# Kernel tuning notes

Measured on AMD Instinct MI355X. Metric: run time of the kernel, lower is better.

The kernel has to match this reference:

```python
import jax, jax.numpy as jnp
import numpy as np

F = 256          # in_features
T = 8            # num_fragment_ion_types = 4 types * 2 charges
N_MONO, N_CLEAV, N_FRAG, N_OUT = 150000, 100000, 80000, 40000
D_CLEAV, D_JOIN, D_COMB = 4, 2, 4


def setup_inputs() -> dict:
    key = jax.random.key(0)
    ks = jax.random.split(key, 14)
    s = 0.05
    return {
        "feature": jax.random.normal(ks[0], (N_MONO, F), jnp.float32),
        "Wg_lost": jax.random.normal(ks[1], (F, 1), jnp.float32) * s,
        "Wg_ret": jax.random.normal(ks[2], (F, 1), jnp.float32) * s,
        "W_ih": jax.random.normal(ks[3], (4 * F, 2 * F), jnp.float32) * s,
        "W_hh": jax.random.normal(ks[4], (4 * F, F), jnp.float32) * s,
        "b_ih": jax.random.normal(ks[5], (4 * F,), jnp.float32) * s,
        "b_hh": jax.random.normal(ks[6], (4 * F,), jnp.float32) * s,
        "Wg_frag": jax.random.normal(ks[7], (F, 1), jnp.float32) * s,
        "W_out": jax.random.normal(ks[8], (F, T), jnp.float32) * s,
        "b_out": jnp.zeros((T,), jnp.float32),
        "lost_src": jax.random.randint(ks[9], (N_CLEAV, D_CLEAV), 0, N_MONO),
        "retained_src": jax.random.randint(ks[10], (N_CLEAV, D_CLEAV), 0, N_MONO),
        "join_src": jax.random.randint(ks[11], (N_FRAG, D_JOIN), 0, N_CLEAV),
        "combine_src": jax.random.randint(ks[12], (N_OUT, D_COMB), 0, N_FRAG),
    }


def _attention_sum(h, Wg):
    # h: [N, D, F] mailbox; gate = Linear(F,1,no bias); softmax over neighbor axis
    logits = jnp.einsum('ndf,fo->ndo', h, Wg)          # [N, D, 1]
    a = jax.nn.softmax(logits, axis=1)
    return jnp.sum(a * h, axis=1)                       # [N, F]


def _lstm(x, W_ih, W_hh, b_ih, b_hh):
    # x: [N, L, I]; torch nn.LSTM gate order i,f,g,o; zero initial state
    N = x.shape[0]
    H = W_hh.shape[1]
    def step(carry, xt):
        h, c = carry
        gates = xt @ W_ih.T + h @ W_hh.T + b_ih + b_hh  # [N, 4H]
        i, f, g, o = jnp.split(gates, 4, axis=-1)
        c = jax.nn.sigmoid(f) * c + jax.nn.sigmoid(i) * jnp.tanh(g)
        h = jax.nn.sigmoid(o) * jnp.tanh(c)
        return (h, c), h
    init = (jnp.zeros((N, H), x.dtype), jnp.zeros((N, H), x.dtype))
    _, hs = jax.lax.scan(step, init, jnp.swapaxes(x, 0, 1))
    return jnp.swapaxes(hs, 0, 1)                       # [N, L, H]


def reference(feature, Wg_lost, Wg_ret, W_ih, W_hh, b_ih, b_hh,
              Wg_frag, W_out, b_out,
              lost_src, retained_src, join_src, combine_src):
    h_lost = _attention_sum(feature[lost_src], Wg_lost)        # [N_cleav, F]
    h_ret = _attention_sum(feature[retained_src], Wg_ret)      # [N_cleav, F]
    cleav = jnp.concatenate([h_lost, h_ret], axis=-1)          # [N_cleav, 2F]
    # Fragment pull over 'join' edges: LSTM over neighbor set, then attention sum
    hs = _lstm(cleav[join_src], W_ih, W_hh, b_ih, b_hh)        # [N_frag, D_join, F]
    frag = _attention_sum(hs, Wg_frag)                         # [N_frag, F]
    # Output head: Linear + ReLU
    frag_out = jax.nn.relu(frag @ W_out + b_out)               # [N_frag, T]
    # copy_u_sum over 'combine' edges: scatter-sum of src outputs to dst
    return frag_out[combine_src].sum(axis=1)                   # [N_out, T]
```

## Files before the change

kernel.cpp:

```cpp
#include <hip/hip_runtime.h>

typedef unsigned short u16;
typedef unsigned int u32;
typedef float f32x4 __attribute__((ext_vector_type(4)));
typedef __bf16 bf16x8 __attribute__((ext_vector_type(8)));

#define F 256
#define T_OUT 8
#define N_MONO 150000
#define N_CLEAV 100000
#define N_FRAG 80000
#define N_OUT 40000
#define M_CLEAV_PAD 100352

static __device__ __forceinline__ u16 f2bf(float f) {
  u32 u = __float_as_uint(f);
  u32 r = (u + 0x7FFFu + ((u >> 16) & 1u)) >> 16;
  return (u16)r;
}
static __device__ __forceinline__ float bf2f(u16 b) {
  return __uint_as_float(((u32)b) << 16);
}
static __device__ __forceinline__ float sigmoidf(float x) {
  return __frcp_rn(1.0f + __expf(-x));
}
static __device__ __forceinline__ float fast_tanh(float x) {
  return 1.0f - 2.0f * __frcp_rn(__expf(2.0f * x) + 1.0f);
}
static __device__ __forceinline__ void async_copy16(const u16* g, const u16* l) {
  __builtin_amdgcn_global_load_lds(
      (const __attribute__((address_space(1))) u32*)g,
      (__attribute__((address_space(3))) u32*)l,
      16, 0, 0);
}

__global__ __launch_bounds__(256) void prep_kernel(
    const float* __restrict__ Wih, const float* __restrict__ Whh,
    const float* __restrict__ bih, const float* __restrict__ bhh,
    u16* __restrict__ Wihb, u16* __restrict__ Whhb, float* __restrict__ bias) {
  int i = blockIdx.x * 256 + threadIdx.x;
  if (i < 1024 * 512) Wihb[i] = f2bf(Wih[i]);
  if (i < 1024 * 256) Whhb[i] = f2bf(Whh[i]);
  if (i < 1024) bias[i] = bih[i] + bhh[i];
}

__global__ __launch_bounds__(256) void attn_pull(
    const float* __restrict__ feat, const float* __restrict__ WgL,
    const float* __restrict__ WgR, const int* __restrict__ lostS,
    const int* __restrict__ retS, u16* __restrict__ cleav) {
  int wave = threadIdx.x >> 6, lane = threadIdx.x & 63;
  int n = blockIdx.x * 4 + wave;
  if (n >= N_CLEAV) return;
  const float4 wgl = *(const float4*)(WgL + lane * 4);
  const float4 wgr = *(const float4*)(WgR + lane * 4);
  for (int sg = 0; sg < 2; ++sg) {
    const int* src = sg ? retS : lostS;
    float4 wg = sg ? wgr : wgl;
    int4 ridx = *(const int4*)(src + n * 4);
    int r[4] = {ridx.x, ridx.y, ridx.z, ridx.w};
    float4 x[4];
#pragma unroll
    for (int d = 0; d < 4; ++d)
      x[d] = *(const float4*)(feat + (size_t)r[d] * F + lane * 4);
    float logit[4];
#pragma unroll
    for (int d = 0; d < 4; ++d) {
      float p = x[d].x * wg.x + x[d].y * wg.y + x[d].z * wg.z + x[d].w * wg.w;
#pragma unroll
      for (int off = 32; off; off >>= 1) p += __shfl_xor(p, off);
      logit[d] = p;
    }
    float mx = fmaxf(fmaxf(logit[0], logit[1]), fmaxf(logit[2], logit[3]));
    float e0 = __expf(logit[0] - mx), e1 = __expf(logit[1] - mx);
    float e2 = __expf(logit[2] - mx), e3 = __expf(logit[3] - mx);
    float inv = 1.f / (e0 + e1 + e2 + e3);
    float a0 = e0 * inv, a1 = e1 * inv, a2 = e2 * inv, a3 = e3 * inv;
    float4 acc;
    acc.x = a0 * x[0].x + a1 * x[1].x + a2 * x[2].x + a3 * x[3].x;
    acc.y = a0 * x[0].y + a1 * x[1].y + a2 * x[2].y + a3 * x[3].y;
    acc.z = a0 * x[0].z + a1 * x[1].z + a2 * x[2].z + a3 * x[3].z;
    acc.w = a0 * x[0].w + a1 * x[1].w + a2 * x[2].w + a3 * x[3].w;
    u32 lo = (u32)f2bf(acc.x) | ((u32)f2bf(acc.y) << 16);
    u32 hi = (u32)f2bf(acc.z) | ((u32)f2bf(acc.w) << 16);
    *(uint2*)(cleav + (size_t)n * 512 + sg * 256 + lane * 4) = make_uint2(lo, hi);
  }
}

template <int EPI, int K>
__global__ __launch_bounds__(256, 4) void gemm_bt(
    const u16* __restrict__ A, const u16* __restrict__ Bw,
    u16* __restrict__ C, const float* __restrict__ bias,
    int nper, int mstrips_valid) {
  __shared__ u16 As[2][128 * 32];
  __shared__ u16 Bs[2][128 * 32];
  const int flat = blockIdx.x;
  const int xcd = flat & 7;
  const int w = flat >> 3;
  const int mstrip = xcd * nper + (w >> 3);
  const int nstrip = w & 7;
  if (mstrip >= mstrips_valid) return;
  const int m0 = mstrip * 128;
  const int n0 = nstrip * 128;

  const int tid = threadIdx.x;
  const int lane = tid & 63;
  const int wave = tid >> 6;
  const int quad = lane >> 4;
  const int l16 = lane & 15;
  const int wm = (wave & 1) * 64;
  const int wn = (wave >> 1) * 64;

  f32x4 acc[4][4];
#pragma unroll
  for (int i = 0; i < 4; i++)
#pragma unroll
    for (int j = 0; j < 4; j++) acc[i][j] = (f32x4){0.f, 0.f, 0.f, 0.f};

  int srow[2], skoff[2], ldsoff[2];
#pragma unroll
  for (int jj = 0; jj < 2; jj++) {
    int c = jj * 256 + tid;
    srow[jj] = c >> 2;
    skoff[jj] = ((c & 3) ^ ((c >> 3) & 3)) * 8;
    ldsoff[jj] = (jj * 256 + (tid & ~63)) * 8;
  }
  const u16* Abase = A + (size_t)m0 * K;
  const u16* Bbase = Bw + (size_t)n0 * K;

  auto stage = [&](int buf, int k0) {
#pragma unroll
    for (int jj = 0; jj < 2; jj++)
      async_copy16(Abase + (size_t)srow[jj] * K + k0 + skoff[jj], &As[buf][ldsoff[jj]]);
#pragma unroll
    for (int jj = 0; jj < 2; jj++)
      async_copy16(Bbase + (size_t)srow[jj] * K + k0 + skoff[jj], &Bs[buf][ldsoff[jj]]);
  };

  stage(0, 0);
  const int nK = K / 32;
  for (int t = 0; t < nK; ++t) {
    __syncthreads();
    if (t + 1 < nK) stage((t + 1) & 1, (t + 1) * 32);
    const int buf = t & 1;
    bf16x8 af[4], bfr[4];
#pragma unroll
    for (int i = 0; i < 4; i++) {
      int m = wm + i * 16 + l16;
      int jp = quad ^ ((m >> 1) & 3);
      af[i] = *(const bf16x8*)&As[buf][m * 32 + jp * 8];
    }
#pragma unroll
    for (int j = 0; j < 4; j++) {
      int n = wn + j * 16 + l16;
      int jp = quad ^ ((n >> 1) & 3);
      bfr[j] = *(const bf16x8*)&Bs[buf][n * 32 + jp * 8];
    }
#pragma unroll
    for (int i = 0; i < 4; i++)
#pragma unroll
      for (int j = 0; j < 4; j++)
        acc[i][j] = __builtin_amdgcn_mfma_f32_16x16x32_bf16(af[i], bfr[j], acc[i][j], 0, 0, 0);
  }

#pragma unroll
  for (int i = 0; i < 4; i++) {
    int mbase = m0 + wm + i * 16 + quad * 4;
#pragma unroll
    for (int j = 0; j < 4; j++) {
      int n = n0 + wn + j * 16 + l16;
      float badd = (EPI == 0) ? bias[n] : 0.f;
#pragma unroll
      for (int r = 0; r < 4; r++) {
        int m = mbase + r;
        C[(size_t)m * 1024 + n] = f2bf(acc[i][j][r] + badd);
      }
    }
  }
}

__global__ __launch_bounds__(256) void lstm_step1(
    const u16* __restrict__ P, const int* __restrict__ join,
    u16* __restrict__ h1, u16* __restrict__ c1) {
  int wave = threadIdx.x >> 6, lane = threadIdx.x & 63;
  int m = blockIdx.x * 4 + wave;
  if (m >= N_FRAG) return;
  int j0 = join[2 * m];
  const u16* row = P + (size_t)j0 * 1024 + lane * 4;
  ushort4 iv = *(const ushort4*)(row);
  ushort4 gv = *(const ushort4*)(row + 512);
  ushort4 ov = *(const ushort4*)(row + 768);
  const u16* ivp = (const u16*)&iv;
  const u16* gvp = (const u16*)&gv;
  const u16* ovp = (const u16*)&ov;
  ushort4 h4, c4;
  u16* h4p = (u16*)&h4;
  u16* c4p = (u16*)&c4;
#pragma unroll
  for (int k = 0; k < 4; k++) {
    float c = sigmoidf(bf2f(ivp[k])) * fast_tanh(bf2f(gvp[k]));
    float hv = sigmoidf(bf2f(ovp[k])) * fast_tanh(c);
    h4p[k] = f2bf(hv);
    c4p[k] = f2bf(c);
  }
  *(ushort4*)(h1 + (size_t)m * 256 + lane * 4) = h4;
  *(ushort4*)(c1 + (size_t)m * 256 + lane * 4) = c4;
}

__global__ __launch_bounds__(256) void lstm_step2_attn_out(
    const u16* __restrict__ G2, const u16* __restrict__ P,
    const int* __restrict__ join, const u16* __restrict__ c1,
    const u16* __restrict__ h1b, const float* __restrict__ Wg,
    const float* __restrict__ Wout, const float* __restrict__ bout,
    float* __restrict__ frag_out) {
  int wave = threadIdx.x >> 6, lane = threadIdx.x & 63;
  int m = blockIdx.x * 4 + wave;
  if (m >= N_FRAG) return;
  int j1 = join[2 * m + 1];
  const u16* row = G2 + (size_t)m * 1024 + lane * 4;
  const u16* prow = P + (size_t)j1 * 1024 + lane * 4;
  ushort4 iv = *(const ushort4*)(row);
  ushort4 fv = *(const ushort4*)(row + 256);
  ushort4 gv = *(const ushort4*)(row + 512);
  ushort4 ov = *(const ushort4*)(row + 768);
  ushort4 pi = *(const ushort4*)(prow);
  ushort4 pf = *(const ushort4*)(prow + 256);
  ushort4 pg = *(const ushort4*)(prow + 512);
  ushort4 po = *(const ushort4*)(prow + 768);
  ushort4 c4 = *(const ushort4*)(c1 + (size_t)m * 256 + lane * 4);
  ushort4 h4 = *(const ushort4*)(h1b + (size_t)m * 256 + lane * 4);
  float4 wg = *(const float4*)(Wg + lane * 4);
  const u16* ivp = (const u16*)&iv; const u16* pip = (const u16*)&pi;
  const u16* fvp = (const u16*)&fv; const u16* pfp = (const u16*)&pf;
  const u16* gvp = (const u16*)&gv; const u16* pgp = (const u16*)&pg;
  const u16* ovp = (const u16*)&ov; const u16* pop = (const u16*)&po;
  const u16* c4p = (const u16*)&c4;
  const u16* h4p = (const u16*)&h4;
  const float* wgp = (const float*)&wg;

  float h1v[4], h2v[4];
  float p1 = 0.f, p2 = 0.f;
#pragma unroll
  for (int k = 0; k < 4; k++) {
    float gi = bf2f(ivp[k]) + bf2f(pip[k]);
    float gf = bf2f(fvp[k]) + bf2f(pfp[k]);
    float gg = bf2f(gvp[k]) + bf2f(pgp[k]);
    float go = bf2f(ovp[k]) + bf2f(pop[k]);
    float c2 = sigmoidf(gf) * bf2f(c4p[k]) + sigmoidf(gi) * fast_tanh(gg);
    float h2 = sigmoidf(go) * fast_tanh(c2);
    h2v[k] = h2;
    h1v[k] = bf2f(h4p[k]);
    p1 += h1v[k] * wgp[k];
    p2 += h2 * wgp[k];
  }
#pragma unroll
  for (int off = 32; off; off >>= 1) {
    p1 += __shfl_xor(p1, off);
    p2 += __shfl_xor(p2, off);
  }
  float mx = fmaxf(p1, p2);
  float e1 = __expf(p1 - mx), e2 = __expf(p2 - mx);
  float inv = __frcp_rn(e1 + e2);
  float a1 = e1 * inv, a2 = e2 * inv;

  float acc[8];
#pragma unroll
  for (int t = 0; t < 8; t++) acc[t] = 0.f;
#pragma unroll
  for (int k = 0; k < 4; k++) {
    float frag = a1 * h1v[k] + a2 * h2v[k];
    int h = lane * 4 + k;
    float4 w0 = *(const float4*)(Wout + h * 8);
    float4 w1 = *(const float4*)(Wout + h * 8 + 4);
    acc[0] += frag * w0.x; acc[1] += frag * w0.y;
    acc[2] += frag * w0.z; acc[3] += frag * w0.w;
    acc[4] += frag * w1.x; acc[5] += frag * w1.y;
    acc[6] += frag * w1.z; acc[7] += frag * w1.w;
  }
#pragma unroll
  for (int off = 32; off; off >>= 1)
#pragma unroll
    for (int t = 0; t < 8; t++) acc[t] += __shfl_xor(acc[t], off);
  if (lane == 0) {
    float4 o0, o1;
    o0.x = fmaxf(acc[0] + bout[0], 0.f);
    o0.y = fmaxf(acc[1] + bout[1], 0.f);
    o0.z = fmaxf(acc[2] + bout[2], 0.f);
    o0.w = fmaxf(acc[3] + bout[3], 0.f);
    o1.x = fmaxf(acc[4] + bout[4], 0.f);
    o1.y = fmaxf(acc[5] + bout[5], 0.f);
    o1.z = fmaxf(acc[6] + bout[6], 0.f);
    o1.w = fmaxf(acc[7] + bout[7], 0.f);
    *(float4*)(frag_out + (size_t)m * 8) = o0;
    *(float4*)(frag_out + (size_t)m * 8 + 4) = o1;
  }
}

__global__ __launch_bounds__(256) void scatter_sum(
    const float* __restrict__ frag_out, const int* __restrict__ comb,
    float* __restrict__ out) {
  int tid = blockIdx.x * 256 + threadIdx.x;
  if (tid >= N_OUT * 8) return;
  int n = tid >> 3, t = tid & 7;
  float s = 0.f;
#pragma unroll
  for (int d = 0; d < 4; d++) {
    int f = comb[n * 4 + d];
    s += frag_out[(size_t)f * 8 + t];
  }
  out[tid] = s;
}

extern "C" void kernel_launch(void* const* d_in, const int* in_sizes, int n_in,
                              void* d_out, int out_size, void* d_ws, size_t ws_size,
                              hipStream_t stream) {
  const float* feature = (const float*)d_in[0];
  const float* WgL = (const float*)d_in[1];
  const float* WgR = (const float*)d_in[2];
  const float* Wih = (const float*)d_in[3];
  const float* Whh = (const float*)d_in[4];
  const float* bih = (const float*)d_in[5];
  const float* bhh = (const float*)d_in[6];
  const float* Wgf = (const float*)d_in[7];
  const float* Wout = (const float*)d_in[8];
  const float* bout = (const float*)d_in[9];
  const int* lostS = (const int*)d_in[10];
  const int* retS = (const int*)d_in[11];
  const int* joinS = (const int*)d_in[12];
  const int* combS = (const int*)d_in[13];
  float* out = (float*)d_out;

  char* ws = (char*)d_ws;
  size_t off = 0;
  auto alloc = [&](size_t bytes) -> char* {
    char* p = ws + off;
    off = (off + bytes + 255) & ~(size_t)255;
    return p;
  };
  u16* Wihb = (u16*)alloc((size_t)1024 * 512 * 2);
  u16* Whhb = (u16*)alloc((size_t)1024 * 256 * 2);
  float* bias = (float*)alloc(1024 * 4);
  u16* P = (u16*)alloc((size_t)M_CLEAV_PAD * 1024 * 2);
  u16* h1 = (u16*)alloc((size_t)N_FRAG * 256 * 2);
  u16* c1 = (u16*)alloc((size_t)N_FRAG * 256 * 2);
  float* frag_out = (float*)alloc((size_t)N_FRAG * 8 * 4);
  char* uni = alloc((size_t)M_CLEAV_PAD * 1024 * 2);
  u16* cleav = (u16*)uni;
  u16* gates2 = (u16*)uni;

  prep_kernel<<<2048, 256, 0, stream>>>(Wih, Whh, bih, bhh, Wihb, Whhb, bias);
  attn_pull<<<N_CLEAV / 4, 256, 0, stream>>>(feature, WgL, WgR, lostS, retS, cleav);
  gemm_bt<0, 512><<<784 * 8, 256, 0, stream>>>(cleav, Wihb, P, bias, 98, 784);
  lstm_step1<<<N_FRAG / 4, 256, 0, stream>>>(P, joinS, h1, c1);
  gemm_bt<1, 256><<<632 * 8, 256, 0, stream>>>(h1, Whhb, gates2, nullptr, 79, 625);
  lstm_step2_attn_out<<<N_FRAG / 4, 256, 0, stream>>>(
      gates2, P, joinS, c1, h1, Wgf, Wout, bout, frag_out);
  scatter_sum<<<(N_OUT * 8 + 255) / 256, 256, 0, stream>>>(frag_out, combS, out);
}
```

Baseline: 746.6 us.

## Restructure GEMM to keep weight strip resident in LDS, stream A directly

Result: slower. 862.7 us (+15.6%).

```diff
diff --git a/kernel.cpp b/kernel.cpp
--- a/kernel.cpp
+++ b/kernel.cpp
@@ -12,6 +12,7 @@
 #define N_FRAG 80000
 #define N_OUT 40000
 #define M_CLEAV_PAD 100352
+#define M_FRAG_PAD 80128
 
 static __device__ __forceinline__ u16 f2bf(float f) {
   u32 u = __float_as_uint(f);
@@ -87,28 +88,35 @@
 }
 
 template <int EPI, int K>
-__global__ __launch_bounds__(256, 4) void gemm_bt(
+__global__ __launch_bounds__(256, 3) void gemm_ws(
     const u16* __restrict__ A, const u16* __restrict__ Bw,
     u16* __restrict__ C, const float* __restrict__ bias,
-    int nper, int mstrips_valid) {
-  __shared__ u16 As[2][128 * 32];
-  __shared__ u16 Bs[2][128 * 32];
+    int Gpad, int gvalid) {
+  constexpr int SLABS = K / 32;
+  __shared__ u16 Ws[K * 64];
+
   const int flat = blockIdx.x;
-  const int xcd = flat & 7;
-  const int w = flat >> 3;
-  const int mstrip = xcd * nper + (w >> 3);
-  const int nstrip = w & 7;
-  if (mstrip >= mstrips_valid) return;
-  const int m0 = mstrip * 128;
-  const int n0 = nstrip * 128;
+  const int g = flat % Gpad;
+  const int nstrip = flat / Gpad;
+  if (g >= gvalid) return;
+  const int m0 = g * 256;
+  const int n0 = nstrip * 64;
 
   const int tid = threadIdx.x;
   const int lane = tid & 63;
   const int wave = tid >> 6;
   const int quad = lane >> 4;
   const int l16 = lane & 15;
-  const int wm = (wave & 1) * 64;
-  const int wn = (wave >> 1) * 64;
+
+  {
+    const int lc = (tid & 3) ^ ((tid >> 3) & 3);
+    const u16* src = Bw + (size_t)(n0 + (tid >> 2)) * K + lc * 8;
+    const int dst = (tid & ~63) * 8;
+#pragma unroll
+    for (int s = 0; s < SLABS; ++s)
+      async_copy16(src + s * 32, Ws + s * 2048 + dst);
+  }
+  __syncthreads();
 
   f32x4 acc[4][4];
 #pragma unroll
@@ -116,44 +124,19 @@
 #pragma unroll
     for (int j = 0; j < 4; j++) acc[i][j] = (f32x4){0.f, 0.f, 0.f, 0.f};
 
-  int srow[2], skoff[2], ldsoff[2];
-#pragma unroll
-  for (int jj = 0; jj < 2; jj++) {
-    int c = jj * 256 + tid;
-    srow[jj] = c >> 2;
-    skoff[jj] = ((c & 3) ^ ((c >> 3) & 3)) * 8;
-    ldsoff[jj] = (jj * 256 + (tid & ~63)) * 8;
-  }
-  const u16* Abase = A + (size_t)m0 * K;
-  const u16* Bbase = Bw + (size_t)n0 * K;
-
-  auto stage = [&](int buf, int k0) {
-#pragma unroll
-    for (int jj = 0; jj < 2; jj++)
-      async_copy16(Abase + (size_t)srow[jj] * K + k0 + skoff[jj], &As[buf][ldsoff[jj]]);
-#pragma unroll
-    for (int jj = 0; jj < 2; jj++)
-      async_copy16(Bbase + (size_t)srow[jj] * K + k0 + skoff[jj], &Bs[buf][ldsoff[jj]]);
-  };
-
-  stage(0, 0);
-  const int nK = K / 32;
-  for (int t = 0; t < nK; ++t) {
-    __syncthreads();
-    if (t + 1 < nK) stage((t + 1) & 1, (t + 1) * 32);
-    const int buf = t & 1;
+  const u16* Aw = A + (size_t)(m0 + wave * 64) * K + quad * 8;
+
+#pragma unroll
+  for (int s = 0; s < SLABS; ++s) {
     bf16x8 af[4], bfr[4];
 #pragma unroll
-    for (int i = 0; i < 4; i++) {
-      int m = wm + i * 16 + l16;
-      int jp = quad ^ ((m >> 1) & 3);
-      af[i] = *(const bf16x8*)&As[buf][m * 32 + jp * 8];
-    }
+    for (int i = 0; i < 4; i++)
+      af[i] = *(const bf16x8*)(Aw + (size_t)(i * 16 + l16) * K + s * 32);
 #pragma unroll
     for (int j = 0; j < 4; j++) {
-      int n = wn + j * 16 + l16;
+      int n = j * 16 + l16;
       int jp = quad ^ ((n >> 1) & 3);
-      bfr[j] = *(const bf16x8*)&Bs[buf][n * 32 + jp * 8];
+      bfr[j] = *(const bf16x8*)&Ws[s * 2048 + n * 32 + jp * 8];
     }
 #pragma unroll
     for (int i = 0; i < 4; i++)
@@ -164,10 +147,10 @@
 
 #pragma unroll
   for (int i = 0; i < 4; i++) {
-    int mbase = m0 + wm + i * 16 + quad * 4;
+    int mbase = m0 + wave * 64 + i * 16 + quad * 4;
 #pragma unroll
     for (int j = 0; j < 4; j++) {
-      int n = n0 + wn + j * 16 + l16;
+      int n = n0 + j * 16 + l16;
       float badd = (EPI == 0) ? bias[n] : 0.f;
 #pragma unroll
       for (int r = 0; r < 4; r++) {
@@ -340,7 +323,7 @@
   u16* Whhb = (u16*)alloc((size_t)1024 * 256 * 2);
   float* bias = (float*)alloc(1024 * 4);
   u16* P = (u16*)alloc((size_t)M_CLEAV_PAD * 1024 * 2);
-  u16* h1 = (u16*)alloc((size_t)N_FRAG * 256 * 2);
+  u16* h1 = (u16*)alloc((size_t)M_FRAG_PAD * 256 * 2);
   u16* c1 = (u16*)alloc((size_t)N_FRAG * 256 * 2);
   float* frag_out = (float*)alloc((size_t)N_FRAG * 8 * 4);
   char* uni = alloc((size_t)M_CLEAV_PAD * 1024 * 2);
@@ -349,9 +332,9 @@
 
   prep_kernel<<<2048, 256, 0, stream>>>(Wih, Whh, bih, bhh, Wihb, Whhb, bias);
   attn_pull<<<N_CLEAV / 4, 256, 0, stream>>>(feature, WgL, WgR, lostS, retS, cleav);
-  gemm_bt<0, 512><<<784 * 8, 256, 0, stream>>>(cleav, Wihb, P, bias, 98, 784);
+  gemm_ws<0, 512><<<16 * 392, 256, 0, stream>>>(cleav, Wihb, P, bias, 392, 392);
   lstm_step1<<<N_FRAG / 4, 256, 0, stream>>>(P, joinS, h1, c1);
-  gemm_bt<1, 256><<<632 * 8, 256, 0, stream>>>(h1, Whhb, gates2, nullptr, 79, 625);
+  gemm_ws<1, 256><<<16 * 320, 256, 0, stream>>>(h1, Whhb, gates2, nullptr, 320, 313);
   lstm_step2_attn_out<<<N_FRAG / 4, 256, 0, stream>>>(
       gates2, P, joinS, c1, h1, Wgf, Wout, bout, frag_out);
   scatter_sum<<<(N_OUT * 8 + 255) / 256, 256, 0, stream>>>(frag_out, combS, out);
```
